# Kernel optimization log

Hardware: AMD Instinct MI355X
Metric: run time of the kernel (lower is better)

## Reference

```python
import jax, jax.numpy as jnp
import numpy as np

# Fixed (non-trainable) 3x3 line-feature kernels, ordered j=0..3 as in the torch module
_KERNELS = np.array([
    [[0.0, 0.0, 0.0], [-0.5, 1.0, -0.5], [0.0, 0.0, 0.0]],   # kernel0 (horizontal)
    [[0.0, 0.0, -0.5], [0.0, 1.0, 0.0], [-0.5, 0.0, 0.0]],   # kernel1 (anti-diagonal)
    [[0.0, -0.5, 0.0], [0.0, 1.0, 0.0], [0.0, -0.5, 0.0]],   # kernel2 (vertical)
    [[-0.5, 0.0, 0.0], [0.0, 1.0, 0.0], [0.0, 0.0, -0.5]],   # kernel3 (diagonal)
], dtype=np.float32)

_EPS = 1e-5  # torch InstanceNorm2d default eps


def setup_inputs() -> dict:
    key = jax.random.key(0)
    x = jax.random.normal(key, (32, 4, 512, 512), dtype=jnp.float32)
    return {"x": x}


def reference(x):
    B, C, H, W = x.shape
    kernels = jnp.asarray(_KERNELS)  # [4, 3, 3]
    out = jnp.zeros_like(x)
    for j in range(4):  # fixed small structural loop over 4 distinct kernels
        w = jnp.broadcast_to(kernels[j][None, None], (C, 1, 3, 3))  # depthwise: groups=C
        y = jax.lax.conv_general_dilated(
            x, w,
            window_strides=(1, 1),
            padding=[(1, 1), (1, 1)],
            dimension_numbers=("NCHW", "OIHW", "NCHW"),
            feature_group_count=C,
        )
        out = out + ((y + 1.0) * 0.5) * (float(2 ** j) / 15.0)
    # InstanceNorm2d (no affine): normalize per (b, c) over spatial dims, biased variance
    mean = jnp.mean(out, axis=(2, 3), keepdims=True)
    var = jnp.var(out, axis=(2, 3), keepdims=True)
    return (out - mean) * jax.lax.rsqrt(var + _EPS)
```

## Files before the change

kernel.cpp:

```cpp
#include <hip/hip_runtime.h>


#define H 512
#define W 512
#define PLANES 128
#define ROWBLKS 16
#define ROWS_PER_TY 16

#define WT0 (-8.0f/30.0f)
#define WT1 (-4.0f/30.0f)
#define WT2 (-2.0f/30.0f)
#define WM  (-1.0f/30.0f)

__device__ __forceinline__ void load_row(const float* __restrict__ rowp, int c0, bool valid,
                                         float& l, float4& m, float& r) {
    if (valid) {
        m = *reinterpret_cast<const float4*>(rowp + c0);
        l = (c0 > 0)       ? rowp[c0 - 1] : 0.0f;
        r = (c0 + 4 < W)   ? rowp[c0 + 4] : 0.0f;
    } else {
        l = 0.0f; r = 0.0f; m = make_float4(0.0f, 0.0f, 0.0f, 0.0f);
    }
}

__device__ __forceinline__ float4 conv_row(float al, float4 a, float ar,
                                           float bl, float4 b, float br,
                                           float dl, float4 d, float dr) {
    float4 o;
    o.x = WT0*al  + WT1*a.x + WT2*a.y + WM*bl  + b.x + WM*b.y + WT2*dl  + WT1*d.x + WT0*d.y;
    o.y = WT0*a.x + WT1*a.y + WT2*a.z + WM*b.x + b.y + WM*b.z + WT2*d.x + WT1*d.y + WT0*d.z;
    o.z = WT0*a.y + WT1*a.z + WT2*a.w + WM*b.y + b.z + WM*b.w + WT2*d.y + WT1*d.z + WT0*d.w;
    o.w = WT0*a.z + WT1*a.w + WT2*ar  + WM*b.z + b.w + WM*br  + WT2*d.z + WT1*d.w + WT0*dr;
    return o;
}

__global__ __launch_bounds__(256) void stats_kernel(const float* __restrict__ x,
                                                    float* __restrict__ ws) {
    const int plane  = blockIdx.x >> 4;
    const int rowblk = blockIdx.x & 15;
    const int tid = threadIdx.x;
    const int tx = tid & 127;
    const int ty = tid >> 7;
    const int c0 = tx * 4;
    const int r0 = rowblk * 32 + ty * ROWS_PER_TY;

    const float* __restrict__ p = x + (size_t)plane * H * W;

    float al, ar, bl, br, dl, dr;
    float4 a4, b4, d4;
    load_row(p + (size_t)(r0 - 1) * W, c0, r0 > 0, al, a4, ar);
    load_row(p + (size_t)r0 * W,       c0, true,   bl, b4, br);

    float s = 0.0f, ss = 0.0f;
    for (int r = r0; r < r0 + ROWS_PER_TY; ++r) {
        load_row(p + (size_t)(r + 1) * W, c0, (r + 1) < H, dl, d4, dr);
        float4 o = conv_row(al, a4, ar, bl, b4, br, dl, d4, dr);
        s  += (o.x + o.y) + (o.z + o.w);
        ss += (o.x*o.x + o.y*o.y) + (o.z*o.z + o.w*o.w);
        al = bl; a4 = b4; ar = br;
        bl = dl; b4 = d4; br = dr;
    }

    for (int off = 32; off > 0; off >>= 1) {
        s  += __shfl_down(s,  off);
        ss += __shfl_down(ss, off);
    }
    __shared__ float sh[8];
    const int wid = tid >> 6, lane = tid & 63;
    if (lane == 0) { sh[wid * 2] = s; sh[wid * 2 + 1] = ss; }
    __syncthreads();
    if (tid == 0) {
        float S  = (sh[0] + sh[2]) + (sh[4] + sh[6]);
        float SS = (sh[1] + sh[3]) + (sh[5] + sh[7]);
        atomicAdd(&ws[plane * 2 + 0], S);
        atomicAdd(&ws[plane * 2 + 1], SS);
    }
}

__global__ __launch_bounds__(256) void norm_kernel(const float* __restrict__ x,
                                                   const float* __restrict__ ws,
                                                   float* __restrict__ out) {
    const int plane  = blockIdx.x >> 4;
    const int rowblk = blockIdx.x & 15;
    const int tid = threadIdx.x;
    const int tx = tid & 127;
    const int ty = tid >> 7;
    const int c0 = tx * 4;
    const int r0 = rowblk * 32 + ty * ROWS_PER_TY;

    const float* __restrict__ p = x + (size_t)plane * H * W;
    float* __restrict__ q = out + (size_t)plane * H * W;

    const float invN = 1.0f / (float)(H * W);
    const float mean = ws[plane * 2 + 0] * invN;
    const float var  = ws[plane * 2 + 1] * invN - mean * mean;
    const float rstd = rsqrtf(var + 4e-5f);

    float al, ar, bl, br, dl, dr;
    float4 a4, b4, d4;
    load_row(p + (size_t)(r0 - 1) * W, c0, r0 > 0, al, a4, ar);
    load_row(p + (size_t)r0 * W,       c0, true,   bl, b4, br);

    for (int r = r0; r < r0 + ROWS_PER_TY; ++r) {
        load_row(p + (size_t)(r + 1) * W, c0, (r + 1) < H, dl, d4, dr);
        float4 o = conv_row(al, a4, ar, bl, b4, br, dl, d4, dr);
        float4 y;
        y.x = (o.x - mean) * rstd;
        y.y = (o.y - mean) * rstd;
        y.z = (o.z - mean) * rstd;
        y.w = (o.w - mean) * rstd;
        *reinterpret_cast<float4*>(q + (size_t)r * W + c0) = y;
        al = bl; a4 = b4; ar = br;
        bl = dl; b4 = d4; br = dr;
    }
}

extern "C" void kernel_launch(void* const* d_in, const int* in_sizes, int n_in,
                              void* d_out, int out_size, void* d_ws, size_t ws_size,
                              hipStream_t stream) {
    const float* x = (const float*)d_in[0];
    float* out = (float*)d_out;
    float* ws  = (float*)d_ws;

    hipMemsetAsync(ws, 0, PLANES * 2 * sizeof(float), stream);

    const dim3 grid(PLANES * ROWBLKS);
    const dim3 block(256);
    stats_kernel<<<grid, block, 0, stream>>>(x, ws);
    norm_kernel <<<grid, block, 0, stream>>>(x, ws, out);
}
```

Baseline: 258.5 us.

## Use wavefront shuffles for halo loads, drop atomics and memset, nontemporal stores

Each wavefront now covers half a row and gets its left/right halo values from neighbour lanes by shuffle instead of extra scalar global loads. Only the edge lanes read from memory. Per-block partial sums are written to the workspace without atomics, and the norm kernel reduces the 16 partials per plane, which removes the hipMemsetAsync launch. Output stores become nontemporal and the convolution is refactored to pair terms that share a weight. The cost is extra shuffle instructions and a small reduction step at the start of each norm block.

```diff
diff --git a/kernel.cpp b/kernel.cpp
--- a/kernel.cpp
+++ b/kernel.cpp
@@ -4,56 +4,64 @@
 #define H 512
 #define W 512
 #define PLANES 128
-#define ROWBLKS 16
-#define ROWS_PER_TY 16
+#define NBLOCKS (PLANES * 16)
+
+typedef float vfloat4 __attribute__((ext_vector_type(4)));
 
 #define WT0 (-8.0f/30.0f)
 #define WT1 (-4.0f/30.0f)
 #define WT2 (-2.0f/30.0f)
 #define WM  (-1.0f/30.0f)
 
-__device__ __forceinline__ void load_row(const float* __restrict__ rowp, int c0, bool valid,
-                                         float& l, float4& m, float& r) {
+__device__ __forceinline__ void wload(const float* __restrict__ rowp, int c0, int ch,
+                                      int lane, bool valid,
+                                      float& l, float4& m, float& r) {
+    float lval = 0.0f, rval = 0.0f;
     if (valid) {
         m = *reinterpret_cast<const float4*>(rowp + c0);
-        l = (c0 > 0)       ? rowp[c0 - 1] : 0.0f;
-        r = (c0 + 4 < W)   ? rowp[c0 + 4] : 0.0f;
+        if (lane == 0  && ch > 0)        lval = rowp[ch - 1];
+        if (lane == 63 && ch + 256 < W)  rval = rowp[ch + 256];
     } else {
-        l = 0.0f; r = 0.0f; m = make_float4(0.0f, 0.0f, 0.0f, 0.0f);
+        m = make_float4(0.0f, 0.0f, 0.0f, 0.0f);
     }
+    float fromL = __shfl_up(m.w, 1);
+    float fromR = __shfl_down(m.x, 1);
+    l = (lane == 0)  ? lval : fromL;
+    r = (lane == 63) ? rval : fromR;
 }
 
 __device__ __forceinline__ float4 conv_row(float al, float4 a, float ar,
                                            float bl, float4 b, float br,
                                            float dl, float4 d, float dr) {
     float4 o;
-    o.x = WT0*al  + WT1*a.x + WT2*a.y + WM*bl  + b.x + WM*b.y + WT2*dl  + WT1*d.x + WT0*d.y;
-    o.y = WT0*a.x + WT1*a.y + WT2*a.z + WM*b.x + b.y + WM*b.z + WT2*d.x + WT1*d.y + WT0*d.z;
-    o.z = WT0*a.y + WT1*a.z + WT2*a.w + WM*b.y + b.z + WM*b.w + WT2*d.y + WT1*d.z + WT0*d.w;
-    o.w = WT0*a.z + WT1*a.w + WT2*ar  + WM*b.z + b.w + WM*br  + WT2*d.z + WT1*d.w + WT0*dr;
+    o.x = b.x + WT0*(al  + d.y) + WT1*(a.x + d.x) + WT2*(a.y + dl ) + WM*(bl  + b.y);
+    o.y = b.y + WT0*(a.x + d.z) + WT1*(a.y + d.y) + WT2*(a.z + d.x) + WM*(b.x + b.z);
+    o.z = b.z + WT0*(a.y + d.w) + WT1*(a.z + d.z) + WT2*(a.w + d.y) + WM*(b.y + b.w);
+    o.w = b.w + WT0*(a.z + dr ) + WT1*(a.w + d.w) + WT2*(ar  + d.z) + WM*(b.z + br );
     return o;
 }
 
 __global__ __launch_bounds__(256) void stats_kernel(const float* __restrict__ x,
                                                     float* __restrict__ ws) {
-    const int plane  = blockIdx.x >> 4;
-    const int rowblk = blockIdx.x & 15;
-    const int tid = threadIdx.x;
-    const int tx = tid & 127;
-    const int ty = tid >> 7;
-    const int c0 = tx * 4;
-    const int r0 = rowblk * 32 + ty * ROWS_PER_TY;
+    const int plane = blockIdx.x >> 4;
+    const int slab  = blockIdx.x & 15;
+    const int tid  = threadIdx.x;
+    const int wid  = tid >> 6;
+    const int lane = tid & 63;
+    const int ch = (wid & 1) * 256;
+    const int c0 = ch + lane * 4;
+    const int r0 = slab * 32 + (wid >> 1) * 16;
 
     const float* __restrict__ p = x + (size_t)plane * H * W;
 
     float al, ar, bl, br, dl, dr;
     float4 a4, b4, d4;
-    load_row(p + (size_t)(r0 - 1) * W, c0, r0 > 0, al, a4, ar);
-    load_row(p + (size_t)r0 * W,       c0, true,   bl, b4, br);
+    wload(p + (size_t)(r0 - 1) * W, c0, ch, lane, r0 > 0, al, a4, ar);
+    wload(p + (size_t)r0 * W,       c0, ch, lane, true,   bl, b4, br);
 
     float s = 0.0f, ss = 0.0f;
-    for (int r = r0; r < r0 + ROWS_PER_TY; ++r) {
-        load_row(p + (size_t)(r + 1) * W, c0, (r + 1) < H, dl, d4, dr);
+    for (int r = r0; r < r0 + 16; ++r) {
+        wload(p + (size_t)(r + 1) * W, c0, ch, lane, (r + 1) < H, dl, d4, dr);
         float4 o = conv_row(al, a4, ar, bl, b4, br, dl, d4, dr);
         s  += (o.x + o.y) + (o.z + o.w);
         ss += (o.x*o.x + o.y*o.y) + (o.z*o.z + o.w*o.w);
@@ -66,50 +74,62 @@
         ss += __shfl_down(ss, off);
     }
     __shared__ float sh[8];
-    const int wid = tid >> 6, lane = tid & 63;
     if (lane == 0) { sh[wid * 2] = s; sh[wid * 2 + 1] = ss; }
     __syncthreads();
     if (tid == 0) {
-        float S  = (sh[0] + sh[2]) + (sh[4] + sh[6]);
-        float SS = (sh[1] + sh[3]) + (sh[5] + sh[7]);
-        atomicAdd(&ws[plane * 2 + 0], S);
-        atomicAdd(&ws[plane * 2 + 1], SS);
+        ws[blockIdx.x * 2 + 0] = (sh[0] + sh[2]) + (sh[4] + sh[6]);
+        ws[blockIdx.x * 2 + 1] = (sh[1] + sh[3]) + (sh[5] + sh[7]);
     }
 }
 
 __global__ __launch_bounds__(256) void norm_kernel(const float* __restrict__ x,
                                                    const float* __restrict__ ws,
                                                    float* __restrict__ out) {
-    const int plane  = blockIdx.x >> 4;
-    const int rowblk = blockIdx.x & 15;
-    const int tid = threadIdx.x;
-    const int tx = tid & 127;
-    const int ty = tid >> 7;
-    const int c0 = tx * 4;
-    const int r0 = rowblk * 32 + ty * ROWS_PER_TY;
+    const int plane = blockIdx.x >> 4;
+    const int slab  = blockIdx.x & 15;
+    const int tid  = threadIdx.x;
+    const int wid  = tid >> 6;
+    const int lane = tid & 63;
+    const int ch = (wid & 1) * 256;
+    const int c0 = ch + lane * 4;
+    const int r0 = slab * 32 + (wid >> 1) * 16;
+
+    __shared__ float sb[2];
+    if (tid < 64) {
+        float s = 0.0f, ss = 0.0f;
+        if (lane < 16) {
+            s  = ws[plane * 32 + lane * 2 + 0];
+            ss = ws[plane * 32 + lane * 2 + 1];
+        }
+        for (int off = 8; off > 0; off >>= 1) {
+            s  += __shfl_down(s,  off);
+            ss += __shfl_down(ss, off);
+        }
+        if (lane == 0) { sb[0] = s; sb[1] = ss; }
+    }
+    __syncthreads();
+    const float invN = 1.0f / (float)(H * W);
+    const float mean = sb[0] * invN;
+    const float var  = sb[1] * invN - mean * mean;
+    const float rstd = rsqrtf(var + 4e-5f);
 
     const float* __restrict__ p = x + (size_t)plane * H * W;
     float* __restrict__ q = out + (size_t)plane * H * W;
 
-    const float invN = 1.0f / (float)(H * W);
-    const float mean = ws[plane * 2 + 0] * invN;
-    const float var  = ws[plane * 2 + 1] * invN - mean * mean;
-    const float rstd = rsqrtf(var + 4e-5f);
-
     float al, ar, bl, br, dl, dr;
     float4 a4, b4, d4;
-    load_row(p + (size_t)(r0 - 1) * W, c0, r0 > 0, al, a4, ar);
-    load_row(p + (size_t)r0 * W,       c0, true,   bl, b4, br);
+    wload(p + (size_t)(r0 - 1) * W, c0, ch, lane, r0 > 0, al, a4, ar);
+    wload(p + (size_t)r0 * W,       c0, ch, lane, true,   bl, b4, br);
 
-    for (int r = r0; r < r0 + ROWS_PER_TY; ++r) {
-        load_row(p + (size_t)(r + 1) * W, c0, (r + 1) < H, dl, d4, dr);
+    for (int r = r0; r < r0 + 16; ++r) {
+        wload(p + (size_t)(r + 1) * W, c0, ch, lane, (r + 1) < H, dl, d4, dr);
         float4 o = conv_row(al, a4, ar, bl, b4, br, dl, d4, dr);
-        float4 y;
+        vfloat4 y;
         y.x = (o.x - mean) * rstd;
         y.y = (o.y - mean) * rstd;
         y.z = (o.z - mean) * rstd;
         y.w = (o.w - mean) * rstd;
-        *reinterpret_cast<float4*>(q + (size_t)r * W + c0) = y;
+        __builtin_nontemporal_store(y, reinterpret_cast<vfloat4*>(q + (size_t)r * W + c0));
         al = bl; a4 = b4; ar = br;
         bl = dl; b4 = d4; br = dr;
     }
@@ -122,10 +142,6 @@
     float* out = (float*)d_out;
     float* ws  = (float*)d_ws;
 
-    hipMemsetAsync(ws, 0, PLANES * 2 * sizeof(float), stream);
-
-    const dim3 grid(PLANES * ROWBLKS);
-    const dim3 block(256);
-    stats_kernel<<<grid, block, 0, stream>>>(x, ws);
-    norm_kernel <<<grid, block, 0, stream>>>(x, ws, out);
+    stats_kernel<<<dim3(NBLOCKS), dim3(256), 0, stream>>>(x, ws);
+    norm_kernel <<<dim3(NBLOCKS), dim3(256), 0, stream>>>(x, ws, out);
 }
```

Measured after the change: 251.5 us. -2.7%, faster.
